# Performance work log

Measured on AMD Instinct MI355X. Metric: run time of the kernel, lower is better.

## Reference

```python
import jax, jax.numpy as jnp
import numpy as np

B, S, D, H = 2, 2048, 1024, 16
NUM_BUCKETS, MAX_DISTANCE = 32, 128


def _relative_position_bucket(relative_position, num_buckets=NUM_BUCKETS, max_distance=MAX_DISTANCE):
    # bidirectional bucketing as in T5
    nb = num_buckets // 2
    n = -relative_position
    ret = (n < 0).astype(jnp.int32) * nb
    n = jnp.abs(n)
    max_exact = nb // 2
    is_small = n < max_exact
    val_if_large = max_exact + (
        jnp.log(jnp.maximum(n, 1).astype(jnp.float32) / max_exact)
        / np.log(max_distance / max_exact)
        * (nb - max_exact)
    ).astype(jnp.int32)
    val_if_large = jnp.minimum(val_if_large, nb - 1)
    return ret + jnp.where(is_small, n, val_if_large)


def setup_inputs() -> dict:
    key = jax.random.key(0)
    ks = jax.random.split(key, 6)
    scale = 1.0 / np.sqrt(D)
    hidden_states = jax.random.normal(ks[0], (B, S, D), dtype=jnp.float32)
    mask = jnp.ones((B, S), dtype=jnp.int32)
    Wq = jax.random.normal(ks[1], (D, D), dtype=jnp.float32) * scale
    Wk = jax.random.normal(ks[2], (D, D), dtype=jnp.float32) * scale
    Wv = jax.random.normal(ks[3], (D, D), dtype=jnp.float32) * scale
    Wo = jax.random.normal(ks[4], (D, D), dtype=jnp.float32) * scale
    rel_bias = jax.random.normal(ks[5], (NUM_BUCKETS, H), dtype=jnp.float32) * 0.02
    return {"hidden_states": hidden_states, "mask": mask,
            "Wq": Wq, "Wk": Wk, "Wv": Wv, "Wo": Wo, "rel_bias": rel_bias}


def reference(hidden_states, mask, Wq, Wk, Wv, Wo, rel_bias):
    b, s, d = hidden_states.shape
    h = H
    d_kv = d // h
    # projections (no bias) -> [b, h, s, d_kv]
    q = (hidden_states @ Wq).reshape(b, s, h, d_kv).transpose(0, 2, 1, 3)
    k = (hidden_states @ Wk).reshape(b, s, h, d_kv).transpose(0, 2, 1, 3)
    v = (hidden_states @ Wv).reshape(b, s, h, d_kv).transpose(0, 2, 1, 3)
    scores = jnp.einsum('bhqd,bhkd->bhqk', q, k) / jnp.sqrt(jnp.float32(d_kv))
    # relative position bias: bucket lookup, [1, h, s, s]
    pos = jnp.arange(s)
    relative_position = pos[None, :] - pos[:, None]  # memory - context
    bucket = _relative_position_bucket(relative_position)
    bias = rel_bias[bucket].transpose(2, 0, 1)[None]  # [1, h, s, s]
    scores = scores + bias
    scores = jnp.where(mask[:, None, None, :] == 0, -1e9, scores)
    attn_weights = jax.nn.softmax(scores, axis=-1)
    context = jnp.einsum('bhqk,bhkd->bhqd', attn_weights, v)
    context = context.transpose(0, 2, 1, 3).reshape(b, s, d)
    output = context @ Wo
    return (output, attn_weights)
```

## Files before the change

### kernel.cpp

```cpp
#include <hip/hip_runtime.h>
#include <stdint.h>

#define BB 2
#define SS 2048
#define DD 1024
#define HH 16
#define DKV 64
#define BH (BB*HH)
#define MROWS (BB*SS)

typedef __attribute__((ext_vector_type(8))) short bf16x8;
typedef __attribute__((ext_vector_type(4))) float f32x4;

#define MFMA16 __builtin_amdgcn_mfma_f32_16x16x32_bf16

__device__ inline short f2bf(float x) {
    union { float f; unsigned u; } v; v.f = x;
    unsigned r = (v.u + 0x7FFFu + ((v.u >> 16) & 1u)) >> 16;
    return (short)r;
}
__device__ inline float bf2f(short h) {
    union { unsigned u; float f; } v; v.u = ((unsigned)(unsigned short)h) << 16;
    return v.f;
}

__global__ __launch_bounds__(256) void cast_split_kernel(
    const float* __restrict__ src, short* __restrict__ hi, short* __restrict__ lo, int n)
{
    int i = (blockIdx.x * 256 + threadIdx.x) * 4;
    if (i >= n) return;
    float4 v = *(const float4*)(src + i);
    short h0 = f2bf(v.x), h1 = f2bf(v.y), h2 = f2bf(v.z), h3 = f2bf(v.w);
    short l0 = f2bf(v.x - bf2f(h0)), l1 = f2bf(v.y - bf2f(h1));
    short l2 = f2bf(v.z - bf2f(h2)), l3 = f2bf(v.w - bf2f(h3));
    *(short4*)(hi + i) = make_short4(h0, h1, h2, h3);
    *(short4*)(lo + i) = make_short4(l0, l1, l2, l3);
}

__global__ void transpose_split_kernel(
    const float* __restrict__ src, short* __restrict__ hi, short* __restrict__ lo, int with_lo)
{
    __shared__ float tile[32][33];
    int bx = blockIdx.x * 32, by = blockIdx.y * 32;
    int tx = threadIdx.x, ty = threadIdx.y;
    for (int i = ty; i < 32; i += 8)
        tile[i][tx] = src[(size_t)(by + i) * DD + bx + tx];
    __syncthreads();
    for (int i = ty; i < 32; i += 8) {
        float v = tile[tx][i];
        short h = f2bf(v);
        size_t off = (size_t)(bx + i) * DD + by + tx;
        hi[off] = h;
        if (with_lo) lo[off] = f2bf(v - bf2f(h));
    }
}

__global__ __launch_bounds__(256) void bias_table_kernel(
    const float* __restrict__ rel_bias, float* __restrict__ btab)
{
    int t = blockIdx.x * 256 + threadIdx.x;
    if (t >= HH * 4096) return;
    int h = t >> 12, idx = t & 4095;
    int delta = idx - 2048;
    int n = -delta;
    int ret = 0;
    if (n < 0) { ret = 16; n = -n; }
    int bucket;
    if (n < 8) bucket = ret + n;
    else {
        int m = 0;
        m += (n >= 12); m += (n >= 16); m += (n >= 23); m += (n >= 32);
        m += (n >= 46); m += (n >= 64); m += (n >= 91); m += (n >= 128);
        int val = 8 + m; if (val > 15) val = 15;
        bucket = ret + val;
    }
    btab[t] = rel_bias[bucket * HH + h];
}

__global__ __launch_bounds__(256) void gemm_split_qk_kernel(
    const short* __restrict__ Ah, const short* __restrict__ Al,
    const short* __restrict__ Bh, const short* __restrict__ Bl,
    short* __restrict__ Qh, short* __restrict__ Ql,
    short* __restrict__ Kh, short* __restrict__ Kl)
{
    __shared__ short sAh[128*32], sAl[128*32], sBh[128*32], sBl[128*32];
    int tid = threadIdx.x;
    int w = tid >> 6, lane = tid & 63, col = lane & 15, quad = lane >> 4;
    int wr = w >> 1, wc = w & 1;
    int bm0 = blockIdx.y * 128, bn0 = blockIdx.x * 128;

    f32x4 acc[4][4];
#pragma unroll
    for (int i = 0; i < 4; ++i)
#pragma unroll
        for (int j = 0; j < 4; ++j) acc[i][j] = (f32x4){0.f,0.f,0.f,0.f};

    for (int k0 = 0; k0 < DD; k0 += 32) {
#pragma unroll
        for (int c = tid; c < 512; c += 256) {
            int row = c >> 2, cg = (c & 3) * 8;
            size_t ga = (size_t)(bm0 + row) * DD + k0 + cg;
            size_t gb = (size_t)(bn0 + row) * DD + k0 + cg;
            *(bf16x8*)&sAh[row*32+cg] = *(const bf16x8*)(Ah + ga);
            *(bf16x8*)&sAl[row*32+cg] = *(const bf16x8*)(Al + ga);
            *(bf16x8*)&sBh[row*32+cg] = *(const bf16x8*)(Bh + gb);
            *(bf16x8*)&sBl[row*32+cg] = *(const bf16x8*)(Bl + gb);
        }
        __syncthreads();
        bf16x8 ah[4], al[4], bh[4], bl[4];
#pragma unroll
        for (int i = 0; i < 4; ++i) {
            int ra = (wr*64 + i*16 + col)*32 + quad*8;
            int rb = (wc*64 + i*16 + col)*32 + quad*8;
            ah[i] = *(bf16x8*)&sAh[ra];
            al[i] = *(bf16x8*)&sAl[ra];
            bh[i] = *(bf16x8*)&sBh[rb];
            bl[i] = *(bf16x8*)&sBl[rb];
        }
#pragma unroll
        for (int i = 0; i < 4; ++i)
#pragma unroll
            for (int j = 0; j < 4; ++j) {
                acc[i][j] = MFMA16(ah[i], bh[j], acc[i][j], 0, 0, 0);
                acc[i][j] = MFMA16(al[i], bh[j], acc[i][j], 0, 0, 0);
                acc[i][j] = MFMA16(ah[i], bl[j], acc[i][j], 0, 0, 0);
            }
        __syncthreads();
    }

#pragma unroll
    for (int i = 0; i < 4; ++i)
#pragma unroll
        for (int j = 0; j < 4; ++j)
#pragma unroll
            for (int r = 0; r < 4; ++r) {
                int gm = bm0 + wr*64 + i*16 + quad*4 + r;
                int gn = bn0 + wc*64 + j*16 + col;
                float v = acc[i][j][r];
                int b = gm >> 11, s = gm & 2047;
                int hh = (gn >> 6) & 15, d = gn & 63;
                size_t off = ((size_t)(b*HH + hh) * SS + s) * DKV + d;
                if (gn < 1024) {
                    v *= 0.125f;
                    short hv = f2bf(v);
                    Qh[off] = hv; Ql[off] = f2bf(v - bf2f(hv));
                } else {
                    short hv = f2bf(v);
                    Kh[off] = hv; Kl[off] = f2bf(v - bf2f(hv));
                }
            }
}

__global__ __launch_bounds__(256) void gemm_plain_kernel(
    const short* __restrict__ A, const short* __restrict__ Bt,
    short* __restrict__ vt_out, float* __restrict__ f_out, int mode)
{
    __shared__ short sA[128*32], sB[128*32];
    int tid = threadIdx.x;
    int w = tid >> 6, lane = tid & 63, col = lane & 15, quad = lane >> 4;
    int wr = w >> 1, wc = w & 1;
    int bm0 = blockIdx.y * 128, bn0 = blockIdx.x * 128;

    f32x4 acc[4][4];
#pragma unroll
    for (int i = 0; i < 4; ++i)
#pragma unroll
        for (int j = 0; j < 4; ++j) acc[i][j] = (f32x4){0.f,0.f,0.f,0.f};

    for (int k0 = 0; k0 < DD; k0 += 32) {
#pragma unroll
        for (int c = tid; c < 512; c += 256) {
            int row = c >> 2, cg = (c & 3) * 8;
            *(bf16x8*)&sA[row*32+cg] = *(const bf16x8*)(A  + (size_t)(bm0 + row) * DD + k0 + cg);
            *(bf16x8*)&sB[row*32+cg] = *(const bf16x8*)(Bt + (size_t)(bn0 + row) * DD + k0 + cg);
        }
        __syncthreads();
        bf16x8 af[4], bf[4];
#pragma unroll
        for (int i = 0; i < 4; ++i) {
            af[i] = *(bf16x8*)&sA[(wr*64 + i*16 + col)*32 + quad*8];
            bf[i] = *(bf16x8*)&sB[(wc*64 + i*16 + col)*32 + quad*8];
        }
#pragma unroll
        for (int i = 0; i < 4; ++i)
#pragma unroll
            for (int j = 0; j < 4; ++j)
                acc[i][j] = MFMA16(af[i], bf[j], acc[i][j], 0, 0, 0);
        __syncthreads();
    }

#pragma unroll
    for (int i = 0; i < 4; ++i)
#pragma unroll
        for (int j = 0; j < 4; ++j)
#pragma unroll
            for (int r = 0; r < 4; ++r) {
                int gm = bm0 + wr*64 + i*16 + quad*4 + r;
                int gn = bn0 + wc*64 + j*16 + col;
                float v = acc[i][j][r];
                if (mode == 0) {
                    int b = gm >> 11, s = gm & 2047;
                    int hh = (gn >> 6) & 15, d = gn & 63;
                    vt_out[((size_t)(b*HH + hh) * DKV + d) * SS + s] = f2bf(v);
                } else {
                    f_out[(size_t)gm * DD + gn] = v;
                }
            }
}

__global__ __launch_bounds__(256) void attn_kernel(
    const short* __restrict__ Qh, const short* __restrict__ Ql,
    const short* __restrict__ Kh, const short* __restrict__ Kl,
    const short* __restrict__ Vt, const float* __restrict__ btab_all,
    const int* __restrict__ mask, float* __restrict__ attn_out,
    short* __restrict__ ctx)
{
    __shared__ short Pt[4][16*64];
    int qb = blockIdx.x * 64;
    int bh = blockIdx.y;
    int b = bh >> 4, h = bh & 15;
    int tid = threadIdx.x, w = tid >> 6, lane = tid & 63;
    int col = lane & 15, quad = lane >> 4;

    const short* Qhb = Qh + ((size_t)bh * SS + qb) * DKV;
    const short* Qlb = Ql + ((size_t)bh * SS + qb) * DKV;
    const short* Khb = Kh + (size_t)bh * SS * DKV;
    const short* Klb = Kl + (size_t)bh * SS * DKV;
    const short* Vb  = Vt + (size_t)bh * DKV * SS;
    const float* btab = btab_all + h * 4096 + 2048;
    const int* mrow = mask + b * SS;

    int arow = w * 16 + col;
    bf16x8 aqh0 = *(const bf16x8*)(Qhb + arow*64 + quad*8);
    bf16x8 aqh1 = *(const bf16x8*)(Qhb + arow*64 + 32 + quad*8);
    bf16x8 aql0 = *(const bf16x8*)(Qlb + arow*64 + quad*8);
    bf16x8 aql1 = *(const bf16x8*)(Qlb + arow*64 + 32 + quad*8);

    int qg[4];
#pragma unroll
    for (int r = 0; r < 4; ++r) qg[r] = qb + w*16 + quad*4 + r;

    float m_r[4], l_r[4];
#pragma unroll
    for (int r = 0; r < 4; ++r) { m_r[r] = -1e30f; l_r[r] = 0.f; }

    for (int kt = 0; kt < 32; ++kt) {
        int kb = kt * 64;
        float sv[4][4];
#pragma unroll
        for (int nt = 0; nt < 4; ++nt) {
            const short* Kp  = Khb + (size_t)(kb + nt*16 + col) * 64;
            const short* Kpl = Klb + (size_t)(kb + nt*16 + col) * 64;
            bf16x8 kh0 = *(const bf16x8*)(Kp + quad*8);
            bf16x8 kh1 = *(const bf16x8*)(Kp + 32 + quad*8);
            bf16x8 kl0 = *(const bf16x8*)(Kpl + quad*8);
            bf16x8 kl1 = *(const bf16x8*)(Kpl + 32 + quad*8);
            f32x4 acc = (f32x4){0.f,0.f,0.f,0.f};
            acc = MFMA16(aqh0, kh0, acc, 0, 0, 0);
            acc = MFMA16(aqh1, kh1, acc, 0, 0, 0);
            acc = MFMA16(aql0, kh0, acc, 0, 0, 0);
            acc = MFMA16(aql1, kh1, acc, 0, 0, 0);
            acc = MFMA16(aqh0, kl0, acc, 0, 0, 0);
            acc = MFMA16(aqh1, kl1, acc, 0, 0, 0);
            int c = kb + nt*16 + col;
            int mk = mrow[c];
#pragma unroll
            for (int r = 0; r < 4; ++r) {
                float x = acc[r] + btab[c - qg[r]];
                sv[nt][r] = (mk == 0) ? -1e9f : x;
            }
        }
#pragma unroll
        for (int r = 0; r < 4; ++r) {
            float tm = fmaxf(fmaxf(sv[0][r], sv[1][r]), fmaxf(sv[2][r], sv[3][r]));
#pragma unroll
            for (int d = 1; d < 16; d <<= 1) tm = fmaxf(tm, __shfl_xor(tm, d, 64));
            float nm = fmaxf(m_r[r], tm);
            float ts = __expf(sv[0][r]-nm) + __expf(sv[1][r]-nm)
                     + __expf(sv[2][r]-nm) + __expf(sv[3][r]-nm);
#pragma unroll
            for (int d = 1; d < 16; d <<= 1) ts += __shfl_xor(ts, d, 64);
            l_r[r] = l_r[r] * __expf(m_r[r] - nm) + ts;
            m_r[r] = nm;
        }
    }
    float invl[4];
#pragma unroll
    for (int r = 0; r < 4; ++r) invl[r] = 1.0f / l_r[r];

    f32x4 O[4];
#pragma unroll
    for (int d = 0; d < 4; ++d) O[d] = (f32x4){0.f,0.f,0.f,0.f};

    for (int kt = 0; kt < 32; ++kt) {
        int kb = kt * 64;
#pragma unroll
        for (int nt = 0; nt < 4; ++nt) {
            const short* Kp  = Khb + (size_t)(kb + nt*16 + col) * 64;
            const short* Kpl = Klb + (size_t)(kb + nt*16 + col) * 64;
            bf16x8 kh0 = *(const bf16x8*)(Kp + quad*8);
            bf16x8 kh1 = *(const bf16x8*)(Kp + 32 + quad*8);
            bf16x8 kl0 = *(const bf16x8*)(Kpl + quad*8);
            bf16x8 kl1 = *(const bf16x8*)(Kpl + 32 + quad*8);
            f32x4 acc = (f32x4){0.f,0.f,0.f,0.f};
            acc = MFMA16(aqh0, kh0, acc, 0, 0, 0);
            acc = MFMA16(aqh1, kh1, acc, 0, 0, 0);
            acc = MFMA16(aql0, kh0, acc, 0, 0, 0);
            acc = MFMA16(aql1, kh1, acc, 0, 0, 0);
            acc = MFMA16(aqh0, kl0, acc, 0, 0, 0);
            acc = MFMA16(aqh1, kl1, acc, 0, 0, 0);
            int c = kb + nt*16 + col;
            int mk = mrow[c];
#pragma unroll
            for (int r = 0; r < 4; ++r) {
                float x = acc[r] + btab[c - qg[r]];
                x = (mk == 0) ? -1e9f : x;
                float p = __expf(x - m_r[r]) * invl[r];
                attn_out[((size_t)bh * SS + qg[r]) * SS + c] = p;
                Pt[w][(quad*4 + r) * 64 + nt*16 + col] = f2bf(p);
            }
        }
        __syncthreads();
        bf16x8 ap0 = *(bf16x8*)&Pt[w][col*64 + quad*8];
        bf16x8 ap1 = *(bf16x8*)&Pt[w][col*64 + 32 + quad*8];
#pragma unroll
        for (int dt = 0; dt < 4; ++dt) {
            const short* Vp = Vb + (size_t)(dt*16 + col) * SS + kb;
            bf16x8 bv0 = *(const bf16x8*)(Vp + quad*8);
            bf16x8 bv1 = *(const bf16x8*)(Vp + 32 + quad*8);
            O[dt] = MFMA16(ap0, bv0, O[dt], 0, 0, 0);
            O[dt] = MFMA16(ap1, bv1, O[dt], 0, 0, 0);
        }
        __syncthreads();
    }

#pragma unroll
    for (int dt = 0; dt < 4; ++dt)
#pragma unroll
        for (int r = 0; r < 4; ++r) {
            int row = b * SS + qg[r];
            int cc = h * DKV + dt*16 + col;
            ctx[(size_t)row * DD + cc] = f2bf(O[dt][r]);
        }
}

extern "C" void kernel_launch(void* const* d_in, const int* in_sizes, int n_in,
                              void* d_out, int out_size, void* d_ws, size_t ws_size,
                              hipStream_t stream)
{
    const float* hidden   = (const float*)d_in[0];
    const int*   mask     = (const int*)d_in[1];
    const float* Wq       = (const float*)d_in[2];
    const float* Wk       = (const float*)d_in[3];
    const float* Wv       = (const float*)d_in[4];
    const float* Wo       = (const float*)d_in[5];
    const float* rel_bias = (const float*)d_in[6];

    float* out  = (float*)d_out;
    float* attn = out + (size_t)BB * SS * DD;

    char* p = (char*)d_ws;
    auto alloc = [&](size_t bytes) { char* r = p; p += (bytes + 255) & ~(size_t)255; return r; };
    short* Xh    = (short*)alloc((size_t)MROWS * DD * 2);
    short* Xl    = (short*)alloc((size_t)MROWS * DD * 2);
    short* Wqkh  = (short*)alloc((size_t)2048 * DD * 2);
    short* Wqkl  = (short*)alloc((size_t)2048 * DD * 2);
    short* Wvt   = (short*)alloc((size_t)DD * DD * 2);
    short* Wot   = (short*)alloc((size_t)DD * DD * 2);
    short* Qhb   = (short*)alloc((size_t)BH * SS * DKV * 2);
    short* Qlb   = (short*)alloc((size_t)BH * SS * DKV * 2);
    short* Khb   = (short*)alloc((size_t)BH * SS * DKV * 2);
    short* Klb   = (short*)alloc((size_t)BH * SS * DKV * 2);
    short* Vtb   = (short*)alloc((size_t)BH * SS * DKV * 2);
    short* ctx   = (short*)alloc((size_t)MROWS * DD * 2);
    float* btab  = (float*)alloc((size_t)HH * 4096 * 4);

    cast_split_kernel<<<(MROWS * DD / 4 + 255) / 256, 256, 0, stream>>>(hidden, Xh, Xl, MROWS * DD);

    dim3 tb(32, 8), tg(32, 32);
    transpose_split_kernel<<<tg, tb, 0, stream>>>(Wq, Wqkh, Wqkl, 1);
    transpose_split_kernel<<<tg, tb, 0, stream>>>(Wk, Wqkh + (size_t)1024 * DD, Wqkl + (size_t)1024 * DD, 1);
    transpose_split_kernel<<<tg, tb, 0, stream>>>(Wv, Wvt, nullptr, 0);
    transpose_split_kernel<<<tg, tb, 0, stream>>>(Wo, Wot, nullptr, 0);

    bias_table_kernel<<<(HH * 4096) / 256, 256, 0, stream>>>(rel_bias, btab);

    gemm_split_qk_kernel<<<dim3(16, 32), 256, 0, stream>>>(Xh, Xl, Wqkh, Wqkl, Qhb, Qlb, Khb, Klb);

    gemm_plain_kernel<<<dim3(8, 32), 256, 0, stream>>>(Xh, Wvt, Vtb, nullptr, 0);

    attn_kernel<<<dim3(32, 32), 256, 0, stream>>>(Qhb, Qlb, Khb, Klb, Vtb, btab, mask, attn, ctx);

    gemm_plain_kernel<<<dim3(8, 32), 256, 0, stream>>>(ctx, Wot, nullptr, out, 1);
}
```

Before: 1.337 ms.

## Use direct global-to-LDS loads in GEMMs and streamline attention softmax loops

The two GEMM kernels now stage tiles with global_load_lds (16-byte direct-to-LDS loads), with each wave assigned its own source buffer, in place of loading through registers. The attention kernel processes key tiles in pairs so two independent MFMA chains can interleave. It defers the cross-lane max/sum reductions of the first pass to a single merge at the end, and precomputes the bias and output row pointers. It also replaces the block-wide barriers around the per-wave P tile with a block-level fence and sets an occupancy hint of 4 blocks per CU. Dropping the barriers relies on the wave-private LDS region being safe without synchronisation, which risks races if the fence is insufficient.

```diff
diff --git a/kernel.cpp b/kernel.cpp
--- a/kernel.cpp
+++ b/kernel.cpp
@@ -22,6 +22,12 @@
 __device__ inline float bf2f(short h) {
     union { unsigned u; float f; } v; v.u = ((unsigned)(unsigned short)h) << 16;
     return v.f;
+}
+
+__device__ inline void gload_lds16(const short* g, short* l) {
+    __builtin_amdgcn_global_load_lds(
+        (const __attribute__((address_space(1))) void*)g,
+        (__attribute__((address_space(3))) void*)l, 16, 0, 0);
 }
 
 __global__ __launch_bounds__(256) void cast_split_kernel(
@@ -89,6 +95,10 @@
     int wr = w >> 1, wc = w & 1;
     int bm0 = blockIdx.y * 128, bn0 = blockIdx.x * 128;
 
+    const short* gsrc = (w == 0) ? Ah : (w == 1) ? Al : (w == 2) ? Bh : Bl;
+    short* ldst = (w == 0) ? sAh : (w == 1) ? sAl : (w == 2) ? sBh : sBl;
+    int rbase = (w < 2) ? bm0 : bn0;
+
     f32x4 acc[4][4];
 #pragma unroll
     for (int i = 0; i < 4; ++i)
@@ -97,14 +107,10 @@
 
     for (int k0 = 0; k0 < DD; k0 += 32) {
 #pragma unroll
-        for (int c = tid; c < 512; c += 256) {
-            int row = c >> 2, cg = (c & 3) * 8;
-            size_t ga = (size_t)(bm0 + row) * DD + k0 + cg;
-            size_t gb = (size_t)(bn0 + row) * DD + k0 + cg;
-            *(bf16x8*)&sAh[row*32+cg] = *(const bf16x8*)(Ah + ga);
-            *(bf16x8*)&sAl[row*32+cg] = *(const bf16x8*)(Al + ga);
-            *(bf16x8*)&sBh[row*32+cg] = *(const bf16x8*)(Bh + gb);
-            *(bf16x8*)&sBl[row*32+cg] = *(const bf16x8*)(Bl + gb);
+        for (int it = 0; it < 8; ++it) {
+            int ci = it * 64 + lane;
+            int row = ci >> 2, cg = (ci & 3) * 8;
+            gload_lds16(gsrc + (size_t)(rbase + row) * DD + k0 + cg, ldst + it * 512);
         }
         __syncthreads();
         bf16x8 ah[4], al[4], bh[4], bl[4];
@@ -161,6 +167,11 @@
     int wr = w >> 1, wc = w & 1;
     int bm0 = blockIdx.y * 128, bn0 = blockIdx.x * 128;
 
+    int widx = w & 1;
+    const short* gsrc = (w < 2) ? A : Bt;
+    short* ldst = (w < 2) ? sA : sB;
+    int rbase = (w < 2) ? bm0 : bn0;
+
     f32x4 acc[4][4];
 #pragma unroll
     for (int i = 0; i < 4; ++i)
@@ -169,10 +180,10 @@
 
     for (int k0 = 0; k0 < DD; k0 += 32) {
 #pragma unroll
-        for (int c = tid; c < 512; c += 256) {
-            int row = c >> 2, cg = (c & 3) * 8;
-            *(bf16x8*)&sA[row*32+cg] = *(const bf16x8*)(A  + (size_t)(bm0 + row) * DD + k0 + cg);
-            *(bf16x8*)&sB[row*32+cg] = *(const bf16x8*)(Bt + (size_t)(bn0 + row) * DD + k0 + cg);
+        for (int it = 0; it < 4; ++it) {
+            int ci = (widx*4 + it) * 64 + lane;
+            int row = ci >> 2, cg = (ci & 3) * 8;
+            gload_lds16(gsrc + (size_t)(rbase + row) * DD + k0 + cg, ldst + (widx*4 + it) * 512);
         }
         __syncthreads();
         bf16x8 af[4], bf[4];
@@ -208,7 +219,7 @@
             }
 }
 
-__global__ __launch_bounds__(256) void attn_kernel(
+__global__ __launch_bounds__(256, 4) void attn_kernel(
     const short* __restrict__ Qh, const short* __restrict__ Ql,
     const short* __restrict__ Kh, const short* __restrict__ Kl,
     const short* __restrict__ Vt, const float* __restrict__ btab_all,
@@ -237,8 +248,14 @@
     bf16x8 aql1 = *(const bf16x8*)(Qlb + arow*64 + 32 + quad*8);
 
     int qg[4];
-#pragma unroll
-    for (int r = 0; r < 4; ++r) qg[r] = qb + w*16 + quad*4 + r;
+    const float* btr[4];
+    float* arow_out[4];
+#pragma unroll
+    for (int r = 0; r < 4; ++r) {
+        qg[r] = qb + w*16 + quad*4 + r;
+        btr[r] = btab - qg[r];
+        arow_out[r] = attn_out + ((size_t)bh * SS + qg[r]) * SS;
+    }
 
     float m_r[4], l_r[4];
 #pragma unroll
@@ -248,45 +265,61 @@
         int kb = kt * 64;
         float sv[4][4];
 #pragma unroll
-        for (int nt = 0; nt < 4; ++nt) {
-            const short* Kp  = Khb + (size_t)(kb + nt*16 + col) * 64;
-            const short* Kpl = Klb + (size_t)(kb + nt*16 + col) * 64;
-            bf16x8 kh0 = *(const bf16x8*)(Kp + quad*8);
-            bf16x8 kh1 = *(const bf16x8*)(Kp + 32 + quad*8);
-            bf16x8 kl0 = *(const bf16x8*)(Kpl + quad*8);
-            bf16x8 kl1 = *(const bf16x8*)(Kpl + 32 + quad*8);
-            f32x4 acc = (f32x4){0.f,0.f,0.f,0.f};
-            acc = MFMA16(aqh0, kh0, acc, 0, 0, 0);
-            acc = MFMA16(aqh1, kh1, acc, 0, 0, 0);
-            acc = MFMA16(aql0, kh0, acc, 0, 0, 0);
-            acc = MFMA16(aql1, kh1, acc, 0, 0, 0);
-            acc = MFMA16(aqh0, kl0, acc, 0, 0, 0);
-            acc = MFMA16(aqh1, kl1, acc, 0, 0, 0);
-            int c = kb + nt*16 + col;
-            int mk = mrow[c];
+        for (int np = 0; np < 2; ++np) {
+            const short* Kp0  = Khb + (size_t)(kb + np*32 + col) * 64;
+            const short* Kpl0 = Klb + (size_t)(kb + np*32 + col) * 64;
+            const short* Kp1  = Kp0  + 16*64;
+            const short* Kpl1 = Kpl0 + 16*64;
+            bf16x8 kh0a = *(const bf16x8*)(Kp0  + quad*8);
+            bf16x8 kh1a = *(const bf16x8*)(Kp0  + 32 + quad*8);
+            bf16x8 kl0a = *(const bf16x8*)(Kpl0 + quad*8);
+            bf16x8 kl1a = *(const bf16x8*)(Kpl0 + 32 + quad*8);
+            bf16x8 kh0b = *(const bf16x8*)(Kp1  + quad*8);
+            bf16x8 kh1b = *(const bf16x8*)(Kp1  + 32 + quad*8);
+            bf16x8 kl0b = *(const bf16x8*)(Kpl1 + quad*8);
+            bf16x8 kl1b = *(const bf16x8*)(Kpl1 + 32 + quad*8);
+            f32x4 acc0 = (f32x4){0.f,0.f,0.f,0.f};
+            f32x4 acc1 = (f32x4){0.f,0.f,0.f,0.f};
+            acc0 = MFMA16(aqh0, kh0a, acc0, 0, 0, 0); acc1 = MFMA16(aqh0, kh0b, acc1, 0, 0, 0);
+            acc0 = MFMA16(aqh1, kh1a, acc0, 0, 0, 0); acc1 = MFMA16(aqh1, kh1b, acc1, 0, 0, 0);
+            acc0 = MFMA16(aql0, kh0a, acc0, 0, 0, 0); acc1 = MFMA16(aql0, kh0b, acc1, 0, 0, 0);
+            acc0 = MFMA16(aql1, kh1a, acc0, 0, 0, 0); acc1 = MFMA16(aql1, kh1b, acc1, 0, 0, 0);
+            acc0 = MFMA16(aqh0, kl0a, acc0, 0, 0, 0); acc1 = MFMA16(aqh0, kl0b, acc1, 0, 0, 0);
+            acc0 = MFMA16(aqh1, kl1a, acc0, 0, 0, 0); acc1 = MFMA16(aqh1, kl1b, acc1, 0, 0, 0);
+            int c0 = kb + np*32 + col;
+            int mk0 = mrow[c0], mk1 = mrow[c0 + 16];
 #pragma unroll
             for (int r = 0; r < 4; ++r) {
-                float x = acc[r] + btab[c - qg[r]];
-                sv[nt][r] = (mk == 0) ? -1e9f : x;
+                sv[np*2  ][r] = (mk0 == 0) ? -1e9f : acc0[r] + btr[r][c0];
+                sv[np*2+1][r] = (mk1 == 0) ? -1e9f : acc1[r] + btr[r][c0 + 16];
             }
         }
 #pragma unroll
         for (int r = 0; r < 4; ++r) {
             float tm = fmaxf(fmaxf(sv[0][r], sv[1][r]), fmaxf(sv[2][r], sv[3][r]));
-#pragma unroll
-            for (int d = 1; d < 16; d <<= 1) tm = fmaxf(tm, __shfl_xor(tm, d, 64));
             float nm = fmaxf(m_r[r], tm);
-            float ts = __expf(sv[0][r]-nm) + __expf(sv[1][r]-nm)
-                     + __expf(sv[2][r]-nm) + __expf(sv[3][r]-nm);
-#pragma unroll
-            for (int d = 1; d < 16; d <<= 1) ts += __shfl_xor(ts, d, 64);
-            l_r[r] = l_r[r] * __expf(m_r[r] - nm) + ts;
+            l_r[r] = l_r[r] * __expf(m_r[r] - nm)
+                   + __expf(sv[0][r]-nm) + __expf(sv[1][r]-nm)
+                   + __expf(sv[2][r]-nm) + __expf(sv[3][r]-nm);
             m_r[r] = nm;
         }
     }
+
     float invl[4];
 #pragma unroll
-    for (int r = 0; r < 4; ++r) invl[r] = 1.0f / l_r[r];
+    for (int r = 0; r < 4; ++r) {
+        float m = m_r[r], l = l_r[r];
+#pragma unroll
+        for (int d = 1; d < 16; d <<= 1) {
+            float mo = __shfl_xor(m, d, 64);
+            float lo = __shfl_xor(l, d, 64);
+            float nm = fmaxf(m, mo);
+            l = l * __expf(m - nm) + lo * __expf(mo - nm);
+            m = nm;
+        }
+        m_r[r] = m;
+        invl[r] = 1.0f / l;
+    }
 
     f32x4 O[4];
 #pragma unroll
@@ -295,32 +328,42 @@
     for (int kt = 0; kt < 32; ++kt) {
         int kb = kt * 64;
 #pragma unroll
-        for (int nt = 0; nt < 4; ++nt) {
-            const short* Kp  = Khb + (size_t)(kb + nt*16 + col) * 64;
-            const short* Kpl = Klb + (size_t)(kb + nt*16 + col) * 64;
-            bf16x8 kh0 = *(const bf16x8*)(Kp + quad*8);
-            bf16x8 kh1 = *(const bf16x8*)(Kp + 32 + quad*8);
-            bf16x8 kl0 = *(const bf16x8*)(Kpl + quad*8);
-            bf16x8 kl1 = *(const bf16x8*)(Kpl + 32 + quad*8);
-            f32x4 acc = (f32x4){0.f,0.f,0.f,0.f};
-            acc = MFMA16(aqh0, kh0, acc, 0, 0, 0);
-            acc = MFMA16(aqh1, kh1, acc, 0, 0, 0);
-            acc = MFMA16(aql0, kh0, acc, 0, 0, 0);
-            acc = MFMA16(aql1, kh1, acc, 0, 0, 0);
-            acc = MFMA16(aqh0, kl0, acc, 0, 0, 0);
-            acc = MFMA16(aqh1, kl1, acc, 0, 0, 0);
-            int c = kb + nt*16 + col;
-            int mk = mrow[c];
+        for (int np = 0; np < 2; ++np) {
+            const short* Kp0  = Khb + (size_t)(kb + np*32 + col) * 64;
+            const short* Kpl0 = Klb + (size_t)(kb + np*32 + col) * 64;
+            const short* Kp1  = Kp0  + 16*64;
+            const short* Kpl1 = Kpl0 + 16*64;
+            bf16x8 kh0a = *(const bf16x8*)(Kp0  + quad*8);
+            bf16x8 kh1a = *(const bf16x8*)(Kp0  + 32 + quad*8);
+            bf16x8 kl0a = *(const bf16x8*)(Kpl0 + quad*8);
+            bf16x8 kl1a = *(const bf16x8*)(Kpl0 + 32 + quad*8);
+            bf16x8 kh0b = *(const bf16x8*)(Kp1  + quad*8);
+            bf16x8 kh1b = *(const bf16x8*)(Kp1  + 32 + quad*8);
+            bf16x8 kl0b = *(const bf16x8*)(Kpl1 + quad*8);
+            bf16x8 kl1b = *(const bf16x8*)(Kpl1 + 32 + quad*8);
+            f32x4 acc0 = (f32x4){0.f,0.f,0.f,0.f};
+            f32x4 acc1 = (f32x4){0.f,0.f,0.f,0.f};
+            acc0 = MFMA16(aqh0, kh0a, acc0, 0, 0, 0); acc1 = MFMA16(aqh0, kh0b, acc1, 0, 0, 0);
+            acc0 = MFMA16(aqh1, kh1a, acc0, 0, 0, 0); acc1 = MFMA16(aqh1, kh1b, acc1, 0, 0, 0);
+            acc0 = MFMA16(aql0, kh0a, acc0, 0, 0, 0); acc1 = MFMA16(aql0, kh0b, acc1, 0, 0, 0);
+            acc0 = MFMA16(aql1, kh1a, acc0, 0, 0, 0); acc1 = MFMA16(aql1, kh1b, acc1, 0, 0, 0);
+            acc0 = MFMA16(aqh0, kl0a, acc0, 0, 0, 0); acc1 = MFMA16(aqh0, kl0b, acc1, 0, 0, 0);
+            acc0 = MFMA16(aqh1, kl1a, acc0, 0, 0, 0); acc1 = MFMA16(aqh1, kl1b, acc1, 0, 0, 0);
+            int c0 = kb + np*32 + col;
+            int mk0 = mrow[c0], mk1 = mrow[c0 + 16];
 #pragma unroll
             for (int r = 0; r < 4; ++r) {
-                float x = acc[r] + btab[c - qg[r]];
-                x = (mk == 0) ? -1e9f : x;
-                float p = __expf(x - m_r[r]) * invl[r];
-                attn_out[((size_t)bh * SS + qg[r]) * SS + c] = p;
-                Pt[w][(quad*4 + r) * 64 + nt*16 + col] = f2bf(p);
+                float x0 = (mk0 == 0) ? -1e9f : acc0[r] + btr[r][c0];
+                float p0 = __expf(x0 - m_r[r]) * invl[r];
+                arow_out[r][c0] = p0;
+                Pt[w][(quad*4 + r) * 64 + np*32 + col] = f2bf(p0);
+                float x1 = (mk1 == 0) ? -1e9f : acc1[r] + btr[r][c0 + 16];
+                float p1 = __expf(x1 - m_r[r]) * invl[r];
+                arow_out[r][c0 + 16] = p1;
+                Pt[w][(quad*4 + r) * 64 + np*32 + 16 + col] = f2bf(p1);
             }
         }
-        __syncthreads();
+        __threadfence_block();
         bf16x8 ap0 = *(bf16x8*)&Pt[w][col*64 + quad*8];
         bf16x8 ap1 = *(bf16x8*)&Pt[w][col*64 + 32 + quad*8];
 #pragma unroll
@@ -331,7 +374,6 @@
             O[dt] = MFMA16(ap0, bv0, O[dt], 0, 0, 0);
             O[dt] = MFMA16(ap1, bv1, O[dt], 0, 0, 0);
         }
-        __syncthreads();
     }
 
 #pragma unroll
```

Measured after the change: 1.331 ms. Within noise of the previous version (-0.4%).

## Drop max pass in attention, split KV across waves, add rescale kernel, LDS DMA loads

Applied to the files above, without the earlier changes.

The attention kernel no longer runs a separate pass for the row max and sum. Each wave instead computes unnormalised exp scores with a clamp at 80, writes them to attn_out, and accumulates the row sums and P·V in a single pass. The key range is split between two wave halves of a 512-thread block, and the partial results are merged through shared memory. A new rescale kernel then normalises the stored attention weights using the saved row sums. The GEMMs also switch to global_load_lds direct-to-LDS loads. This removes the recomputation of QK^T but rewrites the 537 MB attention matrix, and it relies on the score range staying bounded, since the clamp alters results for large logits.

```diff
diff --git a/kernel.cpp b/kernel.cpp
--- a/kernel.cpp
+++ b/kernel.cpp
@@ -22,6 +22,12 @@
 __device__ inline float bf2f(short h) {
     union { unsigned u; float f; } v; v.u = ((unsigned)(unsigned short)h) << 16;
     return v.f;
+}
+
+__device__ inline void gload_lds16(const short* g, short* l) {
+    __builtin_amdgcn_global_load_lds(
+        (const __attribute__((address_space(1))) void*)g,
+        (__attribute__((address_space(3))) void*)l, 16, 0, 0);
 }
 
 __global__ __launch_bounds__(256) void cast_split_kernel(
@@ -89,6 +95,10 @@
     int wr = w >> 1, wc = w & 1;
     int bm0 = blockIdx.y * 128, bn0 = blockIdx.x * 128;
 
+    const short* gsrc = (w == 0) ? Ah : (w == 1) ? Al : (w == 2) ? Bh : Bl;
+    short* ldst = (w == 0) ? sAh : (w == 1) ? sAl : (w == 2) ? sBh : sBl;
+    int rbase = (w < 2) ? bm0 : bn0;
+
     f32x4 acc[4][4];
 #pragma unroll
     for (int i = 0; i < 4; ++i)
@@ -97,14 +107,10 @@
 
     for (int k0 = 0; k0 < DD; k0 += 32) {
 #pragma unroll
-        for (int c = tid; c < 512; c += 256) {
-            int row = c >> 2, cg = (c & 3) * 8;
-            size_t ga = (size_t)(bm0 + row) * DD + k0 + cg;
-            size_t gb = (size_t)(bn0 + row) * DD + k0 + cg;
-            *(bf16x8*)&sAh[row*32+cg] = *(const bf16x8*)(Ah + ga);
-            *(bf16x8*)&sAl[row*32+cg] = *(const bf16x8*)(Al + ga);
-            *(bf16x8*)&sBh[row*32+cg] = *(const bf16x8*)(Bh + gb);
-            *(bf16x8*)&sBl[row*32+cg] = *(const bf16x8*)(Bl + gb);
+        for (int it = 0; it < 8; ++it) {
+            int ci = it * 64 + lane;
+            int row = ci >> 2, cg = (ci & 3) * 8;
+            gload_lds16(gsrc + (size_t)(rbase + row) * DD + k0 + cg, ldst + it * 512);
         }
         __syncthreads();
         bf16x8 ah[4], al[4], bh[4], bl[4];
@@ -161,6 +167,11 @@
     int wr = w >> 1, wc = w & 1;
     int bm0 = blockIdx.y * 128, bn0 = blockIdx.x * 128;
 
+    int widx = w & 1;
+    const short* gsrc = (w < 2) ? A : Bt;
+    short* ldst = (w < 2) ? sA : sB;
+    int rbase = (w < 2) ? bm0 : bn0;
+
     f32x4 acc[4][4];
 #pragma unroll
     for (int i = 0; i < 4; ++i)
@@ -169,10 +180,10 @@
 
     for (int k0 = 0; k0 < DD; k0 += 32) {
 #pragma unroll
-        for (int c = tid; c < 512; c += 256) {
-            int row = c >> 2, cg = (c & 3) * 8;
-            *(bf16x8*)&sA[row*32+cg] = *(const bf16x8*)(A  + (size_t)(bm0 + row) * DD + k0 + cg);
-            *(bf16x8*)&sB[row*32+cg] = *(const bf16x8*)(Bt + (size_t)(bn0 + row) * DD + k0 + cg);
+        for (int it = 0; it < 4; ++it) {
+            int ci = (widx*4 + it) * 64 + lane;
+            int row = ci >> 2, cg = (ci & 3) * 8;
+            gload_lds16(gsrc + (size_t)(rbase + row) * DD + k0 + cg, ldst + (widx*4 + it) * 512);
         }
         __syncthreads();
         bf16x8 af[4], bf[4];
@@ -208,19 +219,21 @@
             }
 }
 
-__global__ __launch_bounds__(256) void attn_kernel(
+__global__ __launch_bounds__(512, 8) void attn_kernel(
     const short* __restrict__ Qh, const short* __restrict__ Ql,
     const short* __restrict__ Kh, const short* __restrict__ Kl,
     const short* __restrict__ Vt, const float* __restrict__ btab_all,
     const int* __restrict__ mask, float* __restrict__ attn_out,
-    short* __restrict__ ctx)
-{
-    __shared__ short Pt[4][16*64];
+    short* __restrict__ ctx, float* __restrict__ larr)
+{
+    __shared__ short Pt[8][1024];
+    __shared__ float lsm[4][16];
     int qb = blockIdx.x * 64;
     int bh = blockIdx.y;
     int b = bh >> 4, h = bh & 15;
     int tid = threadIdx.x, w = tid >> 6, lane = tid & 63;
     int col = lane & 15, quad = lane >> 4;
+    int g = w & 3, half = w >> 2;
 
     const short* Qhb = Qh + ((size_t)bh * SS + qb) * DKV;
     const short* Qlb = Ql + ((size_t)bh * SS + qb) * DKV;
@@ -230,23 +243,31 @@
     const float* btab = btab_all + h * 4096 + 2048;
     const int* mrow = mask + b * SS;
 
-    int arow = w * 16 + col;
+    int arow = g * 16 + col;
     bf16x8 aqh0 = *(const bf16x8*)(Qhb + arow*64 + quad*8);
     bf16x8 aqh1 = *(const bf16x8*)(Qhb + arow*64 + 32 + quad*8);
     bf16x8 aql0 = *(const bf16x8*)(Qlb + arow*64 + quad*8);
     bf16x8 aql1 = *(const bf16x8*)(Qlb + arow*64 + 32 + quad*8);
 
     int qg[4];
-#pragma unroll
-    for (int r = 0; r < 4; ++r) qg[r] = qb + w*16 + quad*4 + r;
-
-    float m_r[4], l_r[4];
-#pragma unroll
-    for (int r = 0; r < 4; ++r) { m_r[r] = -1e30f; l_r[r] = 0.f; }
-
-    for (int kt = 0; kt < 32; ++kt) {
+    const float* btr[4];
+    float* arow_out[4];
+#pragma unroll
+    for (int r = 0; r < 4; ++r) {
+        qg[r] = qb + g*16 + quad*4 + r;
+        btr[r] = btab - qg[r];
+        arow_out[r] = attn_out + ((size_t)bh * SS + qg[r]) * SS;
+    }
+
+    float l_r[4];
+#pragma unroll
+    for (int r = 0; r < 4; ++r) l_r[r] = 0.f;
+    f32x4 O[4];
+#pragma unroll
+    for (int d = 0; d < 4; ++d) O[d] = (f32x4){0.f,0.f,0.f,0.f};
+
+    for (int kt = half*16; kt < half*16 + 16; ++kt) {
         int kb = kt * 64;
-        float sv[4][4];
 #pragma unroll
         for (int nt = 0; nt < 4; ++nt) {
             const short* Kp  = Khb + (size_t)(kb + nt*16 + col) * 64;
@@ -266,61 +287,14 @@
             int mk = mrow[c];
 #pragma unroll
             for (int r = 0; r < 4; ++r) {
-                float x = acc[r] + btab[c - qg[r]];
-                sv[nt][r] = (mk == 0) ? -1e9f : x;
+                float x = fminf(acc[r] + btr[r][c], 80.f);
+                float e = (mk == 0) ? 0.f : __expf(x);
+                arow_out[r][c] = e;
+                l_r[r] += e;
+                Pt[w][(quad*4 + r) * 64 + nt*16 + col] = f2bf(e);
             }
         }
-#pragma unroll
-        for (int r = 0; r < 4; ++r) {
-            float tm = fmaxf(fmaxf(sv[0][r], sv[1][r]), fmaxf(sv[2][r], sv[3][r]));
-#pragma unroll
-            for (int d = 1; d < 16; d <<= 1) tm = fmaxf(tm, __shfl_xor(tm, d, 64));
-            float nm = fmaxf(m_r[r], tm);
-            float ts = __expf(sv[0][r]-nm) + __expf(sv[1][r]-nm)
-                     + __expf(sv[2][r]-nm) + __expf(sv[3][r]-nm);
-#pragma unroll
-            for (int d = 1; d < 16; d <<= 1) ts += __shfl_xor(ts, d, 64);
-            l_r[r] = l_r[r] * __expf(m_r[r] - nm) + ts;
-            m_r[r] = nm;
-        }
-    }
-    float invl[4];
-#pragma unroll
-    for (int r = 0; r < 4; ++r) invl[r] = 1.0f / l_r[r];
-
-    f32x4 O[4];
-#pragma unroll
-    for (int d = 0; d < 4; ++d) O[d] = (f32x4){0.f,0.f,0.f,0.f};
-
-    for (int kt = 0; kt < 32; ++kt) {
-        int kb = kt * 64;
-#pragma unroll
-        for (int nt = 0; nt < 4; ++nt) {
-            const short* Kp  = Khb + (size_t)(kb + nt*16 + col) * 64;
-            const short* Kpl = Klb + (size_t)(kb + nt*16 + col) * 64;
-            bf16x8 kh0 = *(const bf16x8*)(Kp + quad*8);
-            bf16x8 kh1 = *(const bf16x8*)(Kp + 32 + quad*8);
-            bf16x8 kl0 = *(const bf16x8*)(Kpl + quad*8);
-            bf16x8 kl1 = *(const bf16x8*)(Kpl + 32 + quad*8);
-            f32x4 acc = (f32x4){0.f,0.f,0.f,0.f};
-            acc = MFMA16(aqh0, kh0, acc, 0, 0, 0);
-            acc = MFMA16(aqh1, kh1, acc, 0, 0, 0);
-            acc = MFMA16(aql0, kh0, acc, 0, 0, 0);
-            acc = MFMA16(aql1, kh1, acc, 0, 0, 0);
-            acc = MFMA16(aqh0, kl0, acc, 0, 0, 0);
-            acc = MFMA16(aqh1, kl1, acc, 0, 0, 0);
-            int c = kb + nt*16 + col;
-            int mk = mrow[c];
-#pragma unroll
-            for (int r = 0; r < 4; ++r) {
-                float x = acc[r] + btab[c - qg[r]];
-                x = (mk == 0) ? -1e9f : x;
-                float p = __expf(x - m_r[r]) * invl[r];
-                attn_out[((size_t)bh * SS + qg[r]) * SS + c] = p;
-                Pt[w][(quad*4 + r) * 64 + nt*16 + col] = f2bf(p);
-            }
-        }
-        __syncthreads();
+        __threadfence_block();
         bf16x8 ap0 = *(bf16x8*)&Pt[w][col*64 + quad*8];
         bf16x8 ap1 = *(bf16x8*)&Pt[w][col*64 + 32 + quad*8];
 #pragma unroll
@@ -331,17 +305,59 @@
             O[dt] = MFMA16(ap0, bv0, O[dt], 0, 0, 0);
             O[dt] = MFMA16(ap1, bv1, O[dt], 0, 0, 0);
         }
-        __syncthreads();
-    }
-
-#pragma unroll
-    for (int dt = 0; dt < 4; ++dt)
+    }
+
+#pragma unroll
+    for (int r = 0; r < 4; ++r) {
+#pragma unroll
+        for (int d = 1; d < 16; d <<= 1) l_r[r] += __shfl_xor(l_r[r], d, 64);
+    }
+
+    __syncthreads();
+    float* Osm = (float*)&Pt[0][0];
+    if (half == 1) {
+#pragma unroll
+        for (int dt = 0; dt < 4; ++dt)
+#pragma unroll
+            for (int r = 0; r < 4; ++r)
+                Osm[(g*64 + lane)*16 + dt*4 + r] = O[dt][r];
+        if (col == 0) {
+#pragma unroll
+            for (int r = 0; r < 4; ++r) lsm[g][quad*4 + r] = l_r[r];
+        }
+    }
+    __syncthreads();
+    if (half == 0) {
+        float invl[4];
 #pragma unroll
         for (int r = 0; r < 4; ++r) {
-            int row = b * SS + qg[r];
-            int cc = h * DKV + dt*16 + col;
-            ctx[(size_t)row * DD + cc] = f2bf(O[dt][r]);
-        }
+            float lt = l_r[r] + lsm[g][quad*4 + r];
+            invl[r] = 1.0f / lt;
+            if (col == 0) larr[(size_t)bh * SS + qg[r]] = lt;
+        }
+#pragma unroll
+        for (int dt = 0; dt < 4; ++dt)
+#pragma unroll
+            for (int r = 0; r < 4; ++r) {
+                float o = O[dt][r] + Osm[(g*64 + lane)*16 + dt*4 + r];
+                int row = b * SS + qg[r];
+                int cc = h * DKV + dt*16 + col;
+                ctx[(size_t)row * DD + cc] = f2bf(o * invl[r]);
+            }
+    }
+}
+
+__global__ __launch_bounds__(256) void rescale_kernel(
+    float* __restrict__ attn, const float* __restrict__ larr)
+{
+    int row = blockIdx.x;
+    float invl = 1.0f / larr[row];
+    float4* p = (float4*)(attn + (size_t)row * SS);
+    int t = threadIdx.x;
+    float4 v0 = p[t], v1 = p[t + 256];
+    v0.x *= invl; v0.y *= invl; v0.z *= invl; v0.w *= invl;
+    v1.x *= invl; v1.y *= invl; v1.z *= invl; v1.w *= invl;
+    p[t] = v0; p[t + 256] = v1;
 }
 
 extern "C" void kernel_launch(void* const* d_in, const int* in_sizes, int n_in,
@@ -374,6 +390,7 @@
     short* Vtb   = (short*)alloc((size_t)BH * SS * DKV * 2);
     short* ctx   = (short*)alloc((size_t)MROWS * DD * 2);
     float* btab  = (float*)alloc((size_t)HH * 4096 * 4);
+    float* larr  = (float*)alloc((size_t)BH * SS * 4);
 
     cast_split_kernel<<<(MROWS * DD / 4 + 255) / 256, 256, 0, stream>>>(hidden, Xh, Xl, MROWS * DD);
 
@@ -389,7 +406,9 @@
 
     gemm_plain_kernel<<<dim3(8, 32), 256, 0, stream>>>(Xh, Wvt, Vtb, nullptr, 0);
 
-    attn_kernel<<<dim3(32, 32), 256, 0, stream>>>(Qhb, Qlb, Khb, Klb, Vtb, btab, mask, attn, ctx);
+    attn_kernel<<<dim3(32, 32), 512, 0, stream>>>(Qhb, Qlb, Khb, Klb, Vtb, btab, mask, attn, ctx, larr);
+
+    rescale_kernel<<<BH * SS, 256, 0, stream>>>(attn, larr);
 
     gemm_plain_kernel<<<dim3(8, 32), 256, 0, stream>>>(ctx, Wot, nullptr, out, 1);
 }
```

Measured after the change: 1.602 ms. +19.9%, slower.
